# Performance work log

Hardware: AMD Instinct MI355X
Metric: run time of the kernel (lower is better)

## Reference

```python
import jax, jax.numpy as jnp
import numpy as np
from jax import lax

BN_EPS = 1e-5

def ste_sign(x):
    # sign binarization; forward sign(x), backward identity (matches torch .data trick)
    return x + lax.stop_gradient(jnp.sign(x) - x)

def bconv(x, w, b, stride, padding):
    xb = ste_sign(x)
    wb = ste_sign(w)
    y = lax.conv_general_dilated(xb, wb, window_strides=stride, padding=padding,
                                 dimension_numbers=('NCHW', 'OIHW', 'NCHW'))
    return y + b[None, :, None, None]

def bn_htanh(x, g, be, m, v):
    # inference-mode BatchNorm2d followed by Hardtanh
    scale = g / jnp.sqrt(v + BN_EPS)
    y = (x - m[None, :, None, None]) * scale[None, :, None, None] + be[None, :, None, None]
    return jnp.clip(y, -1.0, 1.0)

def maxpool_w2(x):
    # MaxPool2d kernel (1,2) stride (1,2)
    return lax.reduce_window(x, -jnp.inf, lax.max, (1, 1, 1, 2), (1, 1, 1, 2), 'VALID')


def setup_inputs() -> dict:
    key = jax.random.key(0)
    ks = jax.random.split(key, 32)
    num_classes = 10
    d = {}
    d['x'] = jax.random.normal(ks[0], (8192, 1, 6, 128), dtype=jnp.float32)
    shapes = {
        'w1': (32, 1, 1, 9), 'w2': (64, 32, 1, 3), 'w3': (128, 64, 1, 3), 'w4': (128, 128, 6, 1),
    }
    i = 1
    for name, sh in shapes.items():
        fan_in = sh[1] * sh[2] * sh[3]
        d[name] = jax.random.normal(ks[i], sh, dtype=jnp.float32) / np.sqrt(fan_in); i += 1
    for layer, c in zip((1, 2, 3, 4), (32, 64, 128, 128)):
        d[f'b{layer}'] = jax.random.normal(ks[i], (c,), dtype=jnp.float32) * 0.1; i += 1
        d[f'g{layer}'] = jax.random.uniform(ks[i], (c,), minval=0.5, maxval=1.5, dtype=jnp.float32); i += 1
        d[f'be{layer}'] = jax.random.normal(ks[i], (c,), dtype=jnp.float32) * 0.1; i += 1
        d[f'm{layer}'] = jax.random.normal(ks[i], (c,), dtype=jnp.float32) * 0.1; i += 1
        d[f'v{layer}'] = jax.random.uniform(ks[i], (c,), minval=0.5, maxval=1.5, dtype=jnp.float32); i += 1
    d['wfc'] = jax.random.normal(ks[i], (num_classes, 2048), dtype=jnp.float32) / np.sqrt(2048.0); i += 1
    d['bfc'] = jnp.zeros((num_classes,), dtype=jnp.float32)
    return d


def reference(x, w1, b1, g1, be1, m1, v1, w2, b2, g2, be2, m2, v2,
              w3, b3, g3, be3, m3, v3, w4, b4, g4, be4, m4, v4, wfc, bfc):
    h = bconv(x, w1, b1, (1, 2), [(0, 0), (4, 4)])        # (N,32,6,64)
    h = bn_htanh(h, g1, be1, m1, v1)
    h = maxpool_w2(h)                                      # (N,32,6,32)
    h = bconv(h, w2, b2, (1, 1), [(0, 0), (1, 1)])        # (N,64,6,32)
    h = bn_htanh(h, g2, be2, m2, v2)
    h = bconv(h, w3, b3, (1, 1), [(0, 0), (1, 1)])        # (N,128,6,32)
    h = bn_htanh(h, g3, be3, m3, v3)
    h = maxpool_w2(h)                                      # (N,128,6,16)
    h = bconv(h, w4, b4, (1, 1), [(0, 0), (0, 0)])        # (N,128,1,16)
    h = bn_htanh(h, g4, be4, m4, v4)
    h = h.reshape(h.shape[0], -1)                          # (N,2048)
    return h @ wfc.T + bfc
```

## Files before the change

kernel.cpp:

```cpp
#include <hip/hip_runtime.h>

typedef unsigned int u32;
typedef unsigned long long u64;

#define WS_WP2B 0
#define WS_WP2N 768
#define WS_WP3B 1536
#define WS_WP3N 4608
#define WS_WP4B 7680
#define WS_WP4N 19968
#define WS_SC1  32256
#define WS_SC2  32384
#define WS_SC3  32640
#define WS_SC4  33152
#define WS_TOTAL 33664

#define OFF_XS  0
#define OFF_SW1 832
#define OFF_S1B 1344
#define OFF_S1N 2160
#define OFF_S2B 2976
#define OFF_S2N 4608
#define OFF_S3B 6240
#define OFF_S3N 7776
#define OFF_H4  9312
#define OFF_RED 17504
#define LDS_BYTES 17664

#define DEV __device__ __forceinline__

DEV void acc_word(u32 xb, u32 xn, u32 wb, u32 wn, int& na, int& nm) {
  u32 m = xn & wn;
  u32 d = (xb ^ wb) & m;
  na += __popc(m);
  nm += __popc(d);
}

DEV float bn_htanh_f(float y, float m, float sc, float be) {
  float t = (y - m) * sc + be;
  return fminf(1.0f, fmaxf(-1.0f, t));
}

__global__ void setup_pack(const float* __restrict__ w2, const float* __restrict__ w3,
                           const float* __restrict__ w4,
                           const float* __restrict__ g1, const float* __restrict__ v1,
                           const float* __restrict__ g2, const float* __restrict__ v2,
                           const float* __restrict__ g3, const float* __restrict__ v3,
                           const float* __restrict__ g4, const float* __restrict__ v4,
                           unsigned char* __restrict__ ws) {
  int t = blockIdx.x * 256 + threadIdx.x;
  if (t < 192) {
    int c = t / 3, k = t % 3;
    u32 b = 0, n = 0;
    for (int ci = 0; ci < 32; ++ci) {
      float f = w2[(c * 32 + ci) * 3 + k];
      if (f < 0.0f) b |= 1u << ci;
      if (f != 0.0f) n |= 1u << ci;
    }
    ((u32*)(ws + WS_WP2B))[t] = b;
    ((u32*)(ws + WS_WP2N))[t] = n;
  } else if (t < 960) {
    int i = t - 192;
    int g = i & 1, k = (i >> 1) % 3, c = i / 6;
    u32 b = 0, n = 0;
    for (int x = 0; x < 32; ++x) {
      int ci = g * 32 + x;
      float f = w3[(c * 64 + ci) * 3 + k];
      if (f < 0.0f) b |= 1u << x;
      if (f != 0.0f) n |= 1u << x;
    }
    ((u32*)(ws + WS_WP3B))[i] = b;
    ((u32*)(ws + WS_WP3N))[i] = n;
  } else if (t < 4032) {
    int i = t - 960;
    int g = i & 3, r = (i >> 2) % 6, c = i / 24;
    u32 b = 0, n = 0;
    for (int x = 0; x < 32; ++x) {
      int ci = g * 32 + x;
      float f = w4[(c * 128 + ci) * 6 + r];
      if (f < 0.0f) b |= 1u << x;
      if (f != 0.0f) n |= 1u << x;
    }
    ((u32*)(ws + WS_WP4B))[i] = b;
    ((u32*)(ws + WS_WP4N))[i] = n;
  } else if (t < 4384) {
    int i = t - 4032;
    const float* g; const float* v; float* dst; int c;
    if (i < 32)       { g = g1; v = v1; dst = (float*)(ws + WS_SC1); c = i; }
    else if (i < 96)  { g = g2; v = v2; dst = (float*)(ws + WS_SC2); c = i - 32; }
    else if (i < 224) { g = g3; v = v3; dst = (float*)(ws + WS_SC3); c = i - 96; }
    else              { g = g4; v = v4; dst = (float*)(ws + WS_SC4); c = i - 224; }
    dst[c] = g[c] / sqrtf(v[c] + 1e-5f);
  }
}

__global__ __launch_bounds__(256, 4) void bnn_fused(
    const float* __restrict__ x,  const float* __restrict__ w1,
    const float* __restrict__ b1, const float* __restrict__ m1, const float* __restrict__ be1,
    const float* __restrict__ b2, const float* __restrict__ m2, const float* __restrict__ be2,
    const float* __restrict__ b3, const float* __restrict__ m3, const float* __restrict__ be3,
    const float* __restrict__ b4, const float* __restrict__ m4, const float* __restrict__ be4,
    const float* __restrict__ wfc, const float* __restrict__ bfc,
    const unsigned char* __restrict__ ws, float* __restrict__ out) {
  __shared__ __align__(16) unsigned char L[LDS_BYTES];
  const int t = threadIdx.x;
  const int n = blockIdx.x;
  const int lane = t & 63;

  for (int i = t; i < 6240 / 4; i += 256) ((u32*)L)[i] = 0u;
  __syncthreads();

  for (int i = t; i < 768; i += 256) {
    int r = i >> 7, w = i & 127;
    float v = x[n * 768 + i];
    ((signed char*)L)[OFF_XS + r * 136 + 4 + w] = (signed char)((v > 0.0f) - (v < 0.0f));
  }
  for (int i = t; i < 288; i += 256) {
    float v = w1[i];
    int c = i / 9, k = i - c * 9;
    ((signed char*)L)[OFF_SW1 + c * 16 + k] = (signed char)((v > 0.0f) - (v < 0.0f));
  }
  __syncthreads();

  {
    const int q = t >> 5;
    const int c = t & 31;
    const float b1c = b1[c], m1c = m1[c], be1c = be1[c];
    const float sc1c = ((const float*)(ws + WS_SC1))[c];
    int w1s[9];
#pragma unroll
    for (int k = 0; k < 9; ++k) w1s[k] = ((const signed char*)L)[OFF_SW1 + c * 16 + k];
    for (int i = 0; i < 24; ++i) {
      int pos = q * 24 + i;
      int r = pos >> 5, j = pos & 31;
      const signed char* xp = (const signed char*)L + OFF_XS + r * 136 + 4 * j;
      int xv[11];
#pragma unroll
      for (int u = 0; u < 11; ++u) xv[u] = xp[u];
      int a0 = 0, a1 = 0;
#pragma unroll
      for (int k = 0; k < 9; ++k) { a0 += xv[k] * w1s[k]; a1 += xv[k + 2] * w1s[k]; }
      float t0 = bn_htanh_f((float)a0 + b1c, m1c, sc1c, be1c);
      float t1 = bn_htanh_f((float)a1 + b1c, m1c, sc1c, be1c);
      float tm = fmaxf(t0, t1);
      u64 bb = __ballot(tm < 0.0f);
      u64 nn = __ballot(tm != 0.0f);
      if (lane == 0) {
        ((u32*)(L + OFF_S1B))[r * 34 + j + 1] = (u32)bb;
        ((u32*)(L + OFF_S1N))[r * 34 + j + 1] = (u32)nn;
      } else if (lane == 32) {
        ((u32*)(L + OFF_S1B))[r * 34 + j + 1] = (u32)(bb >> 32);
        ((u32*)(L + OFF_S1N))[r * 34 + j + 1] = (u32)(nn >> 32);
      }
    }
  }
  __syncthreads();

  {
    const int wave = t >> 6;
    const int c = lane;
    const float b2c = b2[c], m2c = m2[c], be2c = be2[c];
    const float sc2c = ((const float*)(ws + WS_SC2))[c];
    u32 wb[3], wn[3];
#pragma unroll
    for (int k = 0; k < 3; ++k) {
      wb[k] = ((const u32*)(ws + WS_WP2B))[c * 3 + k];
      wn[k] = ((const u32*)(ws + WS_WP2N))[c * 3 + k];
    }
    const u32* s1b = (const u32*)(L + OFF_S1B);
    const u32* s1n = (const u32*)(L + OFF_S1N);
    for (int i = 0; i < 48; ++i) {
      int pos = wave * 48 + i;
      int r = pos >> 5, w = pos & 31;
      int na = 0, nm = 0;
#pragma unroll
      for (int k = 0; k < 3; ++k)
        acc_word(s1b[r * 34 + w + k], s1n[r * 34 + w + k], wb[k], wn[k], na, nm);
      float tv = bn_htanh_f((float)(na - 2 * nm) + b2c, m2c, sc2c, be2c);
      u64 bb = __ballot(tv < 0.0f);
      u64 nn = __ballot(tv != 0.0f);
      if (lane == 0) {
        u32* p  = (u32*)(L + OFF_S2B) + (r * 34 + w + 1) * 2;
        u32* pn = (u32*)(L + OFF_S2N) + (r * 34 + w + 1) * 2;
        p[0] = (u32)bb;  p[1] = (u32)(bb >> 32);
        pn[0] = (u32)nn; pn[1] = (u32)(nn >> 32);
      }
    }
  }
  __syncthreads();

  {
    const int wave = t >> 6;
    u32 wb[2][3][2], wn[2][3][2];
    float b3c[2], m3c[2], be3c[2], sc3c[2];
#pragma unroll
    for (int h = 0; h < 2; ++h) {
      int c = h * 64 + lane;
      b3c[h] = b3[c]; m3c[h] = m3[c]; be3c[h] = be3[c];
      sc3c[h] = ((const float*)(ws + WS_SC3))[c];
#pragma unroll
      for (int k = 0; k < 3; ++k) {
        uint2 vb = *(const uint2*)((const u32*)(ws + WS_WP3B) + (c * 3 + k) * 2);
        uint2 vn = *(const uint2*)((const u32*)(ws + WS_WP3N) + (c * 3 + k) * 2);
        wb[h][k][0] = vb.x; wb[h][k][1] = vb.y;
        wn[h][k][0] = vn.x; wn[h][k][1] = vn.y;
      }
    }
    const u32* s2b = (const u32*)(L + OFF_S2B);
    const u32* s2n = (const u32*)(L + OFF_S2N);
    for (int i = 0; i < 24; ++i) {
      int pos = wave * 24 + i;
      int r = pos >> 4, j = pos & 15;
      u32 xb[4][2], xn[4][2];
#pragma unroll
      for (int col = 0; col < 4; ++col) {
        int base = (r * 34 + 2 * j + col) * 2;
        uint2 vb = *(const uint2*)(s2b + base);
        uint2 vn = *(const uint2*)(s2n + base);
        xb[col][0] = vb.x; xb[col][1] = vb.y;
        xn[col][0] = vn.x; xn[col][1] = vn.y;
      }
#pragma unroll
      for (int h = 0; h < 2; ++h) {
        int na0 = 0, nm0 = 0, na1 = 0, nm1 = 0;
#pragma unroll
        for (int col = 0; col < 4; ++col) {
#pragma unroll
          for (int g = 0; g < 2; ++g) {
            if (col < 3) acc_word(xb[col][g], xn[col][g], wb[h][col][g], wn[h][col][g], na0, nm0);
            if (col > 0) acc_word(xb[col][g], xn[col][g], wb[h][col - 1][g], wn[h][col - 1][g], na1, nm1);
          }
        }
        float t0 = bn_htanh_f((float)(na0 - 2 * nm0) + b3c[h], m3c[h], sc3c[h], be3c[h]);
        float t1 = bn_htanh_f((float)(na1 - 2 * nm1) + b3c[h], m3c[h], sc3c[h], be3c[h]);
        float tm = fmaxf(t0, t1);
        u64 bb = __ballot(tm < 0.0f);
        u64 nn = __ballot(tm != 0.0f);
        if (lane == 0) {
          u32* p  = (u32*)(L + OFF_S3B) + (r * 16 + j) * 4 + h * 2;
          u32* pn = (u32*)(L + OFF_S3N) + (r * 16 + j) * 4 + h * 2;
          p[0] = (u32)bb;  p[1] = (u32)(bb >> 32);
          pn[0] = (u32)nn; pn[1] = (u32)(nn >> 32);
        }
      }
    }
  }
  __syncthreads();

  {
    const int c = t >> 1, q8 = (t & 1) * 8;
    const float b4c = b4[c], m4c = m4[c], be4c = be4[c];
    const float sc4c = ((const float*)(ws + WS_SC4))[c];
    int na[8], nm[8];
#pragma unroll
    for (int wi = 0; wi < 8; ++wi) { na[wi] = 0; nm[wi] = 0; }
    const u32* s3b = (const u32*)(L + OFF_S3B);
    const u32* s3n = (const u32*)(L + OFF_S3N);
#pragma unroll
    for (int r = 0; r < 6; ++r) {
      uint4 wbv = *(const uint4*)((const u32*)(ws + WS_WP4B) + (c * 6 + r) * 4);
      uint4 wnv = *(const uint4*)((const u32*)(ws + WS_WP4N) + (c * 6 + r) * 4);
#pragma unroll
      for (int wi = 0; wi < 8; ++wi) {
        int w = q8 + wi;
        uint4 xbv = *(const uint4*)(s3b + (r * 16 + w) * 4);
        uint4 xnv = *(const uint4*)(s3n + (r * 16 + w) * 4);
        acc_word(xbv.x, xnv.x, wbv.x, wnv.x, na[wi], nm[wi]);
        acc_word(xbv.y, xnv.y, wbv.y, wnv.y, na[wi], nm[wi]);
        acc_word(xbv.z, xnv.z, wbv.z, wnv.z, na[wi], nm[wi]);
        acc_word(xbv.w, xnv.w, wbv.w, wnv.w, na[wi], nm[wi]);
      }
    }
#pragma unroll
    for (int wi = 0; wi < 8; ++wi) {
      float tv = bn_htanh_f((float)(na[wi] - 2 * nm[wi]) + b4c, m4c, sc4c, be4c);
      ((float*)(L + OFF_H4))[c * 16 + q8 + wi] = tv;
    }
  }
  __syncthreads();

  {
    const float* h4 = (const float*)(L + OFF_H4);
    float xv[8];
#pragma unroll
    for (int u = 0; u < 8; ++u) xv[u] = h4[t * 8 + u];
    float part[10];
#pragma unroll
    for (int o = 0; o < 10; ++o) {
      const float* wr = wfc + o * 2048 + t * 8;
      float s = 0.0f;
#pragma unroll
      for (int u = 0; u < 8; ++u) s += xv[u] * wr[u];
      part[o] = s;
    }
#pragma unroll
    for (int o = 0; o < 10; ++o) {
      float v = part[o];
#pragma unroll
      for (int s = 32; s >= 1; s >>= 1) v += __shfl_down(v, s, 64);
      part[o] = v;
    }
    const int wave = t >> 6;
    if (lane == 0) {
#pragma unroll
      for (int o = 0; o < 10; ++o) ((float*)(L + OFF_RED))[wave * 10 + o] = part[o];
    }
  }
  __syncthreads();
  if (t < 10) {
    const float* red = (const float*)(L + OFF_RED);
    out[n * 10 + t] = red[t] + red[10 + t] + red[20 + t] + red[30 + t] + bfc[t];
  }
}

extern "C" void kernel_launch(void* const* d_in, const int* in_sizes, int n_in,
                              void* d_out, int out_size, void* d_ws, size_t ws_size,
                              hipStream_t stream) {
  const float* x   = (const float*)d_in[0];
  const float* w1  = (const float*)d_in[1];
  const float* w2  = (const float*)d_in[2];
  const float* w3  = (const float*)d_in[3];
  const float* w4  = (const float*)d_in[4];
  const float* b1  = (const float*)d_in[5];
  const float* g1  = (const float*)d_in[6];
  const float* be1 = (const float*)d_in[7];
  const float* m1  = (const float*)d_in[8];
  const float* v1  = (const float*)d_in[9];
  const float* b2  = (const float*)d_in[10];
  const float* g2  = (const float*)d_in[11];
  const float* be2 = (const float*)d_in[12];
  const float* m2  = (const float*)d_in[13];
  const float* v2  = (const float*)d_in[14];
  const float* b3  = (const float*)d_in[15];
  const float* g3  = (const float*)d_in[16];
  const float* be3 = (const float*)d_in[17];
  const float* m3  = (const float*)d_in[18];
  const float* v3  = (const float*)d_in[19];
  const float* b4  = (const float*)d_in[20];
  const float* g4  = (const float*)d_in[21];
  const float* be4 = (const float*)d_in[22];
  const float* m4  = (const float*)d_in[23];
  const float* v4  = (const float*)d_in[24];
  const float* wfc = (const float*)d_in[25];
  const float* bfc = (const float*)d_in[26];
  unsigned char* ws = (unsigned char*)d_ws;
  float* out = (float*)d_out;

  const int N = in_sizes[0] / 768;

  setup_pack<<<18, 256, 0, stream>>>(w2, w3, w4, g1, v1, g2, v2, g3, v3, g4, v4, ws);
  bnn_fused<<<N, 256, 0, stream>>>(x, w1, b1, m1, be1, b2, m2, be2,
                                   b3, m3, be3, b4, m4, be4, wfc, bfc, ws, out);
}
```

Before: 548.5 us.

## Rewrite BNN kernel with precomputed sign thresholds and bit-packed layer 1

Replaces per-layer BN+hardtanh float evaluation with integer thresholds on the mismatch popcount, precomputed per channel (with edge-column variants for padding) in the setup kernel. Layer 1 becomes bit-packed via ballots instead of int8 multiply-accumulate, nonzero masks for activations are dropped, and each thread computes a 32-channel output word directly instead of a ballot per position. Pooling is done by ANDing neighbouring words. Block size grows to 384 threads and LDS shrinks. The trade-off is reliance on exact threshold equivalence, which assumes activations are never exactly zero after the hardtanh.

New measurement: 622.7 us. 1.14x slower.

```diff
diff --git a/kernel.cpp b/kernel.cpp
--- a/kernel.cpp
+++ b/kernel.cpp
@@ -3,284 +3,268 @@
 typedef unsigned int u32;
 typedef unsigned long long u64;
 
-#define WS_WP2B 0
-#define WS_WP2N 768
-#define WS_WP3B 1536
-#define WS_WP3N 4608
-#define WS_WP4B 7680
-#define WS_WP4N 19968
-#define WS_SC1  32256
-#define WS_SC2  32384
-#define WS_SC3  32640
-#define WS_SC4  33152
-#define WS_TOTAL 33664
-
-#define OFF_XS  0
-#define OFF_SW1 832
-#define OFF_S1B 1344
-#define OFF_S1N 2160
-#define OFF_S2B 2976
-#define OFF_S2N 4608
-#define OFF_S3B 6240
-#define OFF_S3N 7776
-#define OFF_H4  9312
-#define OFF_RED 17504
-#define LDS_BYTES 17664
-
-#define DEV __device__ __forceinline__
-
-DEV void acc_word(u32 xb, u32 xn, u32 wb, u32 wn, int& na, int& nm) {
-  u32 m = xn & wn;
-  u32 d = (xb ^ wb) & m;
-  na += __popc(m);
-  nm += __popc(d);
+#define WQ1  0
+#define WQ2  128
+#define WQ3  896
+#define WQ4  2944
+#define WNA4 9088
+#define WSC4 9216
+
+__device__ __forceinline__ int scanT(int na, float bb, float mm, float sc, float be, int lim) {
+  for (int nm = 0; nm <= lim; ++nm) {
+    float tt = (((float)(na - 2 * nm) + bb) - mm) * sc + be;
+    if (tt < 0.0f) return nm;
+  }
+  return 1 << 20;
 }
 
-DEV float bn_htanh_f(float y, float m, float sc, float be) {
-  float t = (y - m) * sc + be;
-  return fminf(1.0f, fmaxf(-1.0f, t));
+__global__ void setup_pack(
+    const float* __restrict__ w1, const float* __restrict__ w2,
+    const float* __restrict__ w3, const float* __restrict__ w4,
+    const float* __restrict__ b1, const float* __restrict__ g1, const float* __restrict__ be1,
+    const float* __restrict__ m1, const float* __restrict__ v1,
+    const float* __restrict__ b2, const float* __restrict__ g2, const float* __restrict__ be2,
+    const float* __restrict__ m2, const float* __restrict__ v2,
+    const float* __restrict__ b3, const float* __restrict__ g3, const float* __restrict__ be3,
+    const float* __restrict__ m3, const float* __restrict__ v3,
+    const float* __restrict__ g4, const float* __restrict__ v4,
+    u32* __restrict__ ws) {
+  const int t = threadIdx.x;
+  if (t < 32) {
+    const int c = t;
+    u32 wb = 0, wn = 0;
+    for (int k = 0; k < 9; ++k) {
+      float f = w1[c * 9 + k];
+      if (f < 0.0f) wb |= 1u << k;
+      if (f != 0.0f) wn |= 1u << k;
+    }
+    float sc = g1[c] / sqrtf(v1[c] + 1e-5f);
+    u64 pack = 0;
+    for (int v = 0; v <= 9; ++v) {
+      u32 T = 15;
+      for (int p = 0; p <= 9; ++p) {
+        float tt = (((float)(v - 2 * p) + b1[c]) - m1[c]) * sc + be1[c];
+        if (tt < 0.0f) { T = (u32)p; break; }
+      }
+      pack |= (u64)T << (4 * v);
+    }
+    u32* W = ws + WQ1 + c * 4;
+    W[0] = wb | (wn << 16);
+    W[1] = (u32)pack;
+    W[2] = (u32)(pack >> 32);
+    W[3] = 0;
+  } else if (t < 96) {
+    const int c = t - 32;
+    u32 wb[3], wn[3];
+    for (int k = 0; k < 3; ++k) {
+      u32 b = 0, nn = 0;
+      for (int ci = 0; ci < 32; ++ci) {
+        float f = w2[(c * 32 + ci) * 3 + k];
+        if (f < 0.0f) b |= 1u << ci;
+        if (f != 0.0f) nn |= 1u << ci;
+      }
+      wb[k] = b; wn[k] = nn;
+    }
+    float sc = g2[c] / sqrtf(v2[c] + 1e-5f);
+    int naI = __popc(wn[0]) + __popc(wn[1]) + __popc(wn[2]);
+    int naL = __popc(wn[1]) + __popc(wn[2]);
+    int naR = __popc(wn[0]) + __popc(wn[1]);
+    int T0 = scanT(naI, b2[c], m2[c], sc, be2[c], 97);
+    int TL = scanT(naL, b2[c], m2[c], sc, be2[c], 97) + __popc(wb[0] & wn[0]);
+    int TR = scanT(naR, b2[c], m2[c], sc, be2[c], 97) + __popc(wb[2] & wn[2]);
+    u32* W = ws + WQ2 + c * 12;
+    W[0] = wb[0]; W[1] = wn[0]; W[2] = wb[1]; W[3] = wn[1]; W[4] = wb[2]; W[5] = wn[2];
+    W[6] = (u32)T0; W[7] = (u32)TL; W[8] = (u32)TR; W[9] = 0; W[10] = 0; W[11] = 0;
+  } else if (t < 224) {
+    const int c = t - 96;
+    u32 wb[3][2], wn[3][2];
+    for (int k = 0; k < 3; ++k)
+      for (int g = 0; g < 2; ++g) {
+        u32 b = 0, nn = 0;
+        for (int xx = 0; xx < 32; ++xx) {
+          int ci = g * 32 + xx;
+          float f = w3[(c * 64 + ci) * 3 + k];
+          if (f < 0.0f) b |= 1u << xx;
+          if (f != 0.0f) nn |= 1u << xx;
+        }
+        wb[k][g] = b; wn[k][g] = nn;
+      }
+    float sc = g3[c] / sqrtf(v3[c] + 1e-5f);
+    int n0 = __popc(wn[0][0]) + __popc(wn[0][1]);
+    int n1 = __popc(wn[1][0]) + __popc(wn[1][1]);
+    int n2 = __popc(wn[2][0]) + __popc(wn[2][1]);
+    int T0 = scanT(n0 + n1 + n2, b3[c], m3[c], sc, be3[c], 193);
+    int TL = scanT(n1 + n2, b3[c], m3[c], sc, be3[c], 193)
+             + __popc(wb[0][0] & wn[0][0]) + __popc(wb[0][1] & wn[0][1]);
+    int TR = scanT(n0 + n1, b3[c], m3[c], sc, be3[c], 193)
+             + __popc(wb[2][0] & wn[2][0]) + __popc(wb[2][1] & wn[2][1]);
+    u32* W = ws + WQ3 + c * 16;
+    for (int k = 0; k < 3; ++k)
+      for (int g = 0; g < 2; ++g) { W[(k * 2 + g) * 2] = wb[k][g]; W[(k * 2 + g) * 2 + 1] = wn[k][g]; }
+    W[12] = (u32)T0; W[13] = (u32)TL; W[14] = (u32)TR; W[15] = 0;
+  } else if (t < 352) {
+    const int c = t - 224;
+    int na4 = 0;
+    for (int r = 0; r < 6; ++r)
+      for (int g = 0; g < 4; ++g) {
+        u32 b = 0, nn = 0;
+        for (int xx = 0; xx < 32; ++xx) {
+          int ci = g * 32 + xx;
+          float f = w4[(c * 128 + ci) * 6 + r];
+          if (f < 0.0f) b |= 1u << xx;
+          if (f != 0.0f) nn |= 1u << xx;
+        }
+        ws[WQ4 + c * 48 + r * 8 + g] = b;
+        ws[WQ4 + c * 48 + r * 8 + 4 + g] = nn;
+        na4 += __popc(nn);
+      }
+    ((int*)(ws + WNA4))[c] = na4;
+    ((float*)(ws + WSC4))[c] = g4[c] / sqrtf(v4[c] + 1e-5f);
+  }
 }
 
-__global__ void setup_pack(const float* __restrict__ w2, const float* __restrict__ w3,
-                           const float* __restrict__ w4,
-                           const float* __restrict__ g1, const float* __restrict__ v1,
-                           const float* __restrict__ g2, const float* __restrict__ v2,
-                           const float* __restrict__ g3, const float* __restrict__ v3,
-                           const float* __restrict__ g4, const float* __restrict__ v4,
-                           unsigned char* __restrict__ ws) {
-  int t = blockIdx.x * 256 + threadIdx.x;
-  if (t < 192) {
-    int c = t / 3, k = t % 3;
-    u32 b = 0, n = 0;
-    for (int ci = 0; ci < 32; ++ci) {
-      float f = w2[(c * 32 + ci) * 3 + k];
-      if (f < 0.0f) b |= 1u << ci;
-      if (f != 0.0f) n |= 1u << ci;
-    }
-    ((u32*)(ws + WS_WP2B))[t] = b;
-    ((u32*)(ws + WS_WP2N))[t] = n;
-  } else if (t < 960) {
-    int i = t - 192;
-    int g = i & 1, k = (i >> 1) % 3, c = i / 6;
-    u32 b = 0, n = 0;
-    for (int x = 0; x < 32; ++x) {
-      int ci = g * 32 + x;
-      float f = w3[(c * 64 + ci) * 3 + k];
-      if (f < 0.0f) b |= 1u << x;
-      if (f != 0.0f) n |= 1u << x;
-    }
-    ((u32*)(ws + WS_WP3B))[i] = b;
-    ((u32*)(ws + WS_WP3N))[i] = n;
-  } else if (t < 4032) {
-    int i = t - 960;
-    int g = i & 3, r = (i >> 2) % 6, c = i / 24;
-    u32 b = 0, n = 0;
-    for (int x = 0; x < 32; ++x) {
-      int ci = g * 32 + x;
-      float f = w4[(c * 128 + ci) * 6 + r];
-      if (f < 0.0f) b |= 1u << x;
-      if (f != 0.0f) n |= 1u << x;
-    }
-    ((u32*)(ws + WS_WP4B))[i] = b;
-    ((u32*)(ws + WS_WP4N))[i] = n;
-  } else if (t < 4384) {
-    int i = t - 4032;
-    const float* g; const float* v; float* dst; int c;
-    if (i < 32)       { g = g1; v = v1; dst = (float*)(ws + WS_SC1); c = i; }
-    else if (i < 96)  { g = g2; v = v2; dst = (float*)(ws + WS_SC2); c = i - 32; }
-    else if (i < 224) { g = g3; v = v3; dst = (float*)(ws + WS_SC3); c = i - 96; }
-    else              { g = g4; v = v4; dst = (float*)(ws + WS_SC4); c = i - 224; }
-    dst[c] = g[c] / sqrtf(v[c] + 1e-5f);
-  }
-}
-
-__global__ __launch_bounds__(256, 4) void bnn_fused(
-    const float* __restrict__ x,  const float* __restrict__ w1,
-    const float* __restrict__ b1, const float* __restrict__ m1, const float* __restrict__ be1,
-    const float* __restrict__ b2, const float* __restrict__ m2, const float* __restrict__ be2,
-    const float* __restrict__ b3, const float* __restrict__ m3, const float* __restrict__ be3,
+__global__ __launch_bounds__(384) void bnn_fused(
+    const float* __restrict__ x,
     const float* __restrict__ b4, const float* __restrict__ m4, const float* __restrict__ be4,
     const float* __restrict__ wfc, const float* __restrict__ bfc,
-    const unsigned char* __restrict__ ws, float* __restrict__ out) {
-  __shared__ __align__(16) unsigned char L[LDS_BYTES];
+    const u32* __restrict__ ws, float* __restrict__ out) {
+  __shared__ float h4[2048];
+  __shared__ __align__(16) u32 s3b[6 * 16 * 4];
+  __shared__ u32 s1b[6 * 34];
+  __shared__ u32 s2b[6 * 34 * 2];
+  __shared__ float red[40];
+
   const int t = threadIdx.x;
   const int n = blockIdx.x;
   const int lane = t & 63;
-
-  for (int i = t; i < 6240 / 4; i += 256) ((u32*)L)[i] = 0u;
-  __syncthreads();
-
-  for (int i = t; i < 768; i += 256) {
-    int r = i >> 7, w = i & 127;
-    float v = x[n * 768 + i];
-    ((signed char*)L)[OFF_XS + r * 136 + 4 + w] = (signed char)((v > 0.0f) - (v < 0.0f));
-  }
-  for (int i = t; i < 288; i += 256) {
-    float v = w1[i];
-    int c = i / 9, k = i - c * 9;
-    ((signed char*)L)[OFF_SW1 + c * 16 + k] = (signed char)((v > 0.0f) - (v < 0.0f));
-  }
-  __syncthreads();
+  const int wv = t >> 6;
 
   {
-    const int q = t >> 5;
-    const int c = t & 31;
-    const float b1c = b1[c], m1c = m1[c], be1c = be1[c];
-    const float sc1c = ((const float*)(ws + WS_SC1))[c];
-    int w1s[9];
-#pragma unroll
-    for (int k = 0; k < 9; ++k) w1s[k] = ((const signed char*)L)[OFF_SW1 + c * 16 + k];
-    for (int i = 0; i < 24; ++i) {
-      int pos = q * 24 + i;
-      int r = pos >> 5, j = pos & 31;
-      const signed char* xp = (const signed char*)L + OFF_XS + r * 136 + 4 * j;
-      int xv[11];
-#pragma unroll
-      for (int u = 0; u < 11; ++u) xv[u] = xp[u];
-      int a0 = 0, a1 = 0;
-#pragma unroll
-      for (int k = 0; k < 9; ++k) { a0 += xv[k] * w1s[k]; a1 += xv[k + 2] * w1s[k]; }
-      float t0 = bn_htanh_f((float)a0 + b1c, m1c, sc1c, be1c);
-      float t1 = bn_htanh_f((float)a1 + b1c, m1c, sc1c, be1c);
-      float tm = fmaxf(t0, t1);
-      u64 bb = __ballot(tm < 0.0f);
-      u64 nn = __ballot(tm != 0.0f);
-      if (lane == 0) {
-        ((u32*)(L + OFF_S1B))[r * 34 + j + 1] = (u32)bb;
-        ((u32*)(L + OFF_S1N))[r * 34 + j + 1] = (u32)nn;
-      } else if (lane == 32) {
-        ((u32*)(L + OFF_S1B))[r * 34 + j + 1] = (u32)(bb >> 32);
-        ((u32*)(L + OFF_S1N))[r * 34 + j + 1] = (u32)(nn >> 32);
-      }
-    }
+    const float* xp = x + n * 768 + wv * 128;
+    float x0 = xp[lane], x1 = xp[lane + 64];
+    u64 nb0 = __ballot(x0 < 0.0f);
+    u64 nz0 = __ballot(x0 != 0.0f);
+    u64 nb1 = __ballot(x1 < 0.0f);
+    u64 nz1 = __ballot(x1 != 0.0f);
+    u32 B0 = (u32)nb0 << 4, B1 = (u32)(nb0 >> 28), B2 = (u32)(nb0 >> 60) | ((u32)nb1 << 4);
+    u32 B3 = (u32)(nb1 >> 28), B4 = (u32)(nb1 >> 60);
+    u32 N0 = (u32)nz0 << 4, N1 = (u32)(nz0 >> 28), N2 = (u32)(nz0 >> 60) | ((u32)nz1 << 4);
+    u32 N3 = (u32)(nz1 >> 28), N4 = (u32)(nz1 >> 60);
+    int s = lane * 2, k = s >> 5, sh = s & 31;
+    bool k1 = (k & 1) != 0, k2 = (k & 2) != 0;
+    u32 blo = k2 ? (k1 ? B3 : B2) : (k1 ? B1 : B0);
+    u32 bhi = k2 ? (k1 ? B4 : B3) : (k1 ? B2 : B1);
+    u32 nlo = k2 ? (k1 ? N3 : N2) : (k1 ? N1 : N0);
+    u32 nhi = k2 ? (k1 ? N4 : N3) : (k1 ? N2 : N1);
+    u32 xb = (u32)(((((u64)bhi << 32) | blo) >> sh)) & 0x1FF;
+    u32 xn = (u32)(((((u64)nhi << 32) | nlo) >> sh)) & 0x1FF;
+    const uint4* q1 = (const uint4*)(ws + WQ1);
+    u32 word = 0;
+#pragma unroll 8
+    for (int c = 0; c < 32; ++c) {
+      uint4 q = q1[c];
+      u32 wb = q.x & 0x1FF, wn = q.x >> 16;
+      u32 m = xn & wn;
+      u32 v = (u32)__popc(m);
+      int p1 = __popc((xb ^ wb) & m) + 1;
+      u64 P = ((u64)q.z << 32) | q.y;
+      int T = (int)((u32)(P >> (v << 2)) & 15u);
+      word |= ((u32)(T - p1) >> 31) << c;
+    }
+    u32 pooled = word & __shfl_xor(word, 1, 64);
+    if (!(lane & 1)) s1b[wv * 34 + 1 + (lane >> 1)] = pooled;
+    if (lane == 1) s1b[wv * 34] = 0;
+    if (lane == 3) s1b[wv * 34 + 33] = 0;
   }
   __syncthreads();
 
   {
-    const int wave = t >> 6;
-    const int c = lane;
-    const float b2c = b2[c], m2c = m2[c], be2c = be2[c];
-    const float sc2c = ((const float*)(ws + WS_SC2))[c];
-    u32 wb[3], wn[3];
-#pragma unroll
-    for (int k = 0; k < 3; ++k) {
-      wb[k] = ((const u32*)(ws + WS_WP2B))[c * 3 + k];
-      wn[k] = ((const u32*)(ws + WS_WP2N))[c * 3 + k];
-    }
-    const u32* s1b = (const u32*)(L + OFF_S1B);
-    const u32* s1n = (const u32*)(L + OFF_S1N);
-    for (int i = 0; i < 48; ++i) {
-      int pos = wave * 48 + i;
-      int r = pos >> 5, w = pos & 31;
-      int na = 0, nm = 0;
-#pragma unroll
-      for (int k = 0; k < 3; ++k)
-        acc_word(s1b[r * 34 + w + k], s1n[r * 34 + w + k], wb[k], wn[k], na, nm);
-      float tv = bn_htanh_f((float)(na - 2 * nm) + b2c, m2c, sc2c, be2c);
-      u64 bb = __ballot(tv < 0.0f);
-      u64 nn = __ballot(tv != 0.0f);
-      if (lane == 0) {
-        u32* p  = (u32*)(L + OFF_S2B) + (r * 34 + w + 1) * 2;
-        u32* pn = (u32*)(L + OFF_S2N) + (r * 34 + w + 1) * 2;
-        p[0] = (u32)bb;  p[1] = (u32)(bb >> 32);
-        pn[0] = (u32)nn; pn[1] = (u32)(nn >> 32);
-      }
-    }
+    int h = (t >= 192) ? 1 : 0;
+    int hs = __builtin_amdgcn_readfirstlane(h);
+    int pp = t - 192 * h;
+    int r = pp >> 5, w = pp & 31;
+    if (t < 24) {
+      int rr = t >> 2, side = (t >> 1) & 1, g = t & 1;
+      s2b[(rr * 34 + side * 33) * 2 + g] = 0;
+    }
+    u32 X0 = s1b[r * 34 + w], X1 = s1b[r * 34 + w + 1], X2 = s1b[r * 34 + w + 2];
+    bool cL = (w == 0), cR = (w == 31);
+    const u32* q2 = ws + WQ2 + hs * 32 * 12;
+    u32 word = 0;
+#pragma unroll 4
+    for (int i = 0; i < 32; ++i) {
+      const u32* W = q2 + i * 12;
+      int nm1 = __popc((X0 ^ W[0]) & W[1]) + __popc((X1 ^ W[2]) & W[3])
+              + __popc((X2 ^ W[4]) & W[5]) + 1;
+      int T = cL ? (int)W[7] : (cR ? (int)W[8] : (int)W[6]);
+      word |= ((u32)(T - nm1) >> 31) << i;
+    }
+    s2b[(r * 34 + w + 1) * 2 + h] = word;
   }
   __syncthreads();
 
   {
-    const int wave = t >> 6;
-    u32 wb[2][3][2], wn[2][3][2];
-    float b3c[2], m3c[2], be3c[2], sc3c[2];
-#pragma unroll
-    for (int h = 0; h < 2; ++h) {
-      int c = h * 64 + lane;
-      b3c[h] = b3[c]; m3c[h] = m3[c]; be3c[h] = be3[c];
-      sc3c[h] = ((const float*)(ws + WS_SC3))[c];
-#pragma unroll
-      for (int k = 0; k < 3; ++k) {
-        uint2 vb = *(const uint2*)((const u32*)(ws + WS_WP3B) + (c * 3 + k) * 2);
-        uint2 vn = *(const uint2*)((const u32*)(ws + WS_WP3N) + (c * 3 + k) * 2);
-        wb[h][k][0] = vb.x; wb[h][k][1] = vb.y;
-        wn[h][k][0] = vn.x; wn[h][k][1] = vn.y;
-      }
-    }
-    const u32* s2b = (const u32*)(L + OFF_S2B);
-    const u32* s2n = (const u32*)(L + OFF_S2N);
-    for (int i = 0; i < 24; ++i) {
-      int pos = wave * 24 + i;
-      int r = pos >> 4, j = pos & 15;
-      u32 xb[4][2], xn[4][2];
-#pragma unroll
-      for (int col = 0; col < 4; ++col) {
-        int base = (r * 34 + 2 * j + col) * 2;
-        uint2 vb = *(const uint2*)(s2b + base);
-        uint2 vn = *(const uint2*)(s2n + base);
-        xb[col][0] = vb.x; xb[col][1] = vb.y;
-        xn[col][0] = vn.x; xn[col][1] = vn.y;
-      }
-#pragma unroll
-      for (int h = 0; h < 2; ++h) {
-        int na0 = 0, nm0 = 0, na1 = 0, nm1 = 0;
-#pragma unroll
-        for (int col = 0; col < 4; ++col) {
-#pragma unroll
-          for (int g = 0; g < 2; ++g) {
-            if (col < 3) acc_word(xb[col][g], xn[col][g], wb[h][col][g], wn[h][col][g], na0, nm0);
-            if (col > 0) acc_word(xb[col][g], xn[col][g], wb[h][col - 1][g], wn[h][col - 1][g], na1, nm1);
-          }
-        }
-        float t0 = bn_htanh_f((float)(na0 - 2 * nm0) + b3c[h], m3c[h], sc3c[h], be3c[h]);
-        float t1 = bn_htanh_f((float)(na1 - 2 * nm1) + b3c[h], m3c[h], sc3c[h], be3c[h]);
-        float tm = fmaxf(t0, t1);
-        u64 bb = __ballot(tm < 0.0f);
-        u64 nn = __ballot(tm != 0.0f);
-        if (lane == 0) {
-          u32* p  = (u32*)(L + OFF_S3B) + (r * 16 + j) * 4 + h * 2;
-          u32* pn = (u32*)(L + OFF_S3N) + (r * 16 + j) * 4 + h * 2;
-          p[0] = (u32)bb;  p[1] = (u32)(bb >> 32);
-          pn[0] = (u32)nn; pn[1] = (u32)(nn >> 32);
-        }
-      }
+    int h = (t >= 192) ? 1 : 0;
+    int hs = __builtin_amdgcn_readfirstlane(h);
+    int pp = t - 192 * h;
+    int r = pp >> 5, w = pp & 31;
+    const u32* S = s2b + (r * 34 + w) * 2;
+    u32 X0 = S[0], X1 = S[1], X2 = S[2], X3 = S[3], X4 = S[4], X5 = S[5];
+    bool cL = (w == 0), cR = (w == 31);
+    const u32* q3 = ws + WQ3 + hs * 64 * 16;
+    u32 w0 = 0, w1 = 0;
+#pragma unroll 2
+    for (int i = 0; i < 32; ++i) {
+      {
+        const u32* W = q3 + i * 16;
+        int nm1 = __popc((X0 ^ W[0]) & W[1]) + __popc((X1 ^ W[2]) & W[3])
+                + __popc((X2 ^ W[4]) & W[5]) + __popc((X3 ^ W[6]) & W[7])
+                + __popc((X4 ^ W[8]) & W[9]) + __popc((X5 ^ W[10]) & W[11]) + 1;
+        int T = cL ? (int)W[13] : (cR ? (int)W[14] : (int)W[12]);
+        w0 |= ((u32)(T - nm1) >> 31) << i;
+      }
+      {
+        const u32* W = q3 + (i + 32) * 16;
+        int nm1 = __popc((X0 ^ W[0]) & W[1]) + __popc((X1 ^ W[2]) & W[3])
+                + __popc((X2 ^ W[4]) & W[5]) + __popc((X3 ^ W[6]) & W[7])
+                + __popc((X4 ^ W[8]) & W[9]) + __popc((X5 ^ W[10]) & W[11]) + 1;
+        int T = cL ? (int)W[13] : (cR ? (int)W[14] : (int)W[12]);
+        w1 |= ((u32)(T - nm1) >> 31) << i;
+      }
+    }
+    u32 p0 = w0 & __shfl_xor(w0, 1, 64);
+    u32 p1 = w1 & __shfl_xor(w1, 1, 64);
+    if (!(pp & 1)) {
+      int j = w >> 1;
+      s3b[(r * 16 + j) * 4 + h * 2] = p0;
+      s3b[(r * 16 + j) * 4 + h * 2 + 1] = p1;
     }
   }
   __syncthreads();
 
   {
-    const int c = t >> 1, q8 = (t & 1) * 8;
-    const float b4c = b4[c], m4c = m4[c], be4c = be4[c];
-    const float sc4c = ((const float*)(ws + WS_SC4))[c];
-    int na[8], nm[8];
-#pragma unroll
-    for (int wi = 0; wi < 8; ++wi) { na[wi] = 0; nm[wi] = 0; }
-    const u32* s3b = (const u32*)(L + OFF_S3B);
-    const u32* s3n = (const u32*)(L + OFF_S3N);
-#pragma unroll
-    for (int r = 0; r < 6; ++r) {
-      uint4 wbv = *(const uint4*)((const u32*)(ws + WS_WP4B) + (c * 6 + r) * 4);
-      uint4 wnv = *(const uint4*)((const u32*)(ws + WS_WP4N) + (c * 6 + r) * 4);
-#pragma unroll
-      for (int wi = 0; wi < 8; ++wi) {
-        int w = q8 + wi;
-        uint4 xbv = *(const uint4*)(s3b + (r * 16 + w) * 4);
-        uint4 xnv = *(const uint4*)(s3n + (r * 16 + w) * 4);
-        acc_word(xbv.x, xnv.x, wbv.x, wnv.x, na[wi], nm[wi]);
-        acc_word(xbv.y, xnv.y, wbv.y, wnv.y, na[wi], nm[wi]);
-        acc_word(xbv.z, xnv.z, wbv.z, wnv.z, na[wi], nm[wi]);
-        acc_word(xbv.w, xnv.w, wbv.w, wnv.w, na[wi], nm[wi]);
-      }
-    }
-#pragma unroll
-    for (int wi = 0; wi < 8; ++wi) {
-      float tv = bn_htanh_f((float)(na[wi] - 2 * nm[wi]) + b4c, m4c, sc4c, be4c);
-      ((float*)(L + OFF_H4))[c * 16 + q8 + wi] = tv;
-    }
-  }
-  __syncthreads();
-
-  {
-    const float* h4 = (const float*)(L + OFF_H4);
+    const int* na4 = (const int*)(ws + WNA4);
+    const float* sc4 = (const float*)(ws + WSC4);
+    for (int o = t; o < 2048; o += 384) {
+      int c = o >> 4, w = o & 15;
+      const uint4* Wb = (const uint4*)(ws + WQ4 + c * 48);
+      const uint4* X = (const uint4*)(s3b) + w;
+      int nm = 0;
+#pragma unroll
+      for (int r = 0; r < 6; ++r) {
+        uint4 xv = X[r * 16];
+        uint4 bv = Wb[r * 2], nv = Wb[r * 2 + 1];
+        nm += __popc((xv.x ^ bv.x) & nv.x) + __popc((xv.y ^ bv.y) & nv.y)
+            + __popc((xv.z ^ bv.z) & nv.z) + __popc((xv.w ^ bv.w) & nv.w);
+      }
+      float a = (float)(na4[c] - 2 * nm);
+      float tt = ((a + b4[c]) - m4[c]) * sc4[c] + be4[c];
+      h4[o] = fminf(1.0f, fmaxf(-1.0f, tt));
+    }
+  }
+  __syncthreads();
+
+  if (t < 256) {
     float xv[8];
 #pragma unroll
     for (int u = 0; u < 8; ++u) xv[u] = h4[t * 8 + u];
@@ -288,29 +272,25 @@
 #pragma unroll
     for (int o = 0; o < 10; ++o) {
       const float* wr = wfc + o * 2048 + t * 8;
-      float s = 0.0f;
-#pragma unroll
-      for (int u = 0; u < 8; ++u) s += xv[u] * wr[u];
-      part[o] = s;
+      float sAcc = 0.0f;
+#pragma unroll
+      for (int u = 0; u < 8; ++u) sAcc += xv[u] * wr[u];
+      part[o] = sAcc;
     }
 #pragma unroll
     for (int o = 0; o < 10; ++o) {
       float v = part[o];
 #pragma unroll
-      for (int s = 32; s >= 1; s >>= 1) v += __shfl_down(v, s, 64);
+      for (int sft = 32; sft >= 1; sft >>= 1) v += __shfl_down(v, sft, 64);
       part[o] = v;
     }
-    const int wave = t >> 6;
     if (lane == 0) {
 #pragma unroll
-      for (int o = 0; o < 10; ++o) ((float*)(L + OFF_RED))[wave * 10 + o] = part[o];
-    }
-  }
-  __syncthreads();
-  if (t < 10) {
-    const float* red = (const float*)(L + OFF_RED);
-    out[n * 10 + t] = red[t] + red[10 + t] + red[20 + t] + red[30 + t] + bfc[t];
-  }
+      for (int o = 0; o < 10; ++o) red[wv * 10 + o] = part[o];
+    }
+  }
+  __syncthreads();
+  if (t < 10) out[n * 10 + t] = red[t] + red[10 + t] + red[20 + t] + red[30 + t] + bfc[t];
 }
 
 extern "C" void kernel_launch(void* const* d_in, const int* in_sizes, int n_in,
@@ -343,12 +323,15 @@
   const float* v4  = (const float*)d_in[24];
   const float* wfc = (const float*)d_in[25];
   const float* bfc = (const float*)d_in[26];
-  unsigned char* ws = (unsigned char*)d_ws;
+  u32* ws = (u32*)d_ws;
   float* out = (float*)d_out;
 
   const int N = in_sizes[0] / 768;
 
-  setup_pack<<<18, 256, 0, stream>>>(w2, w3, w4, g1, v1, g2, v2, g3, v3, g4, v4, ws);
-  bnn_fused<<<N, 256, 0, stream>>>(x, w1, b1, m1, be1, b2, m2, be2,
-                                   b3, m3, be3, b4, m4, be4, wfc, bfc, ws, out);
+  setup_pack<<<1, 384, 0, stream>>>(w1, w2, w3, w4,
+                                    b1, g1, be1, m1, v1,
+                                    b2, g2, be2, m2, v2,
+                                    b3, g3, be3, m3, v3,
+                                    g4, v4, ws);
+  bnn_fused<<<N, 384, 0, stream>>>(x, b4, m4, be4, wfc, bfc, ws, out);
 }
```
